# Optimization experiments

Measured on AMD Instinct MI355X. Metric: run time of the kernel, lower is better.

The kernel has to match this reference:

```python
import jax, jax.numpy as jnp
import numpy as np

N_NODES = 100000
N_EDGES = 1600000
IN_CH = 128
HID = 128
OUT_CH = 16
N_GRAPHS = 64


def setup_inputs() -> dict:
    key = jax.random.key(0)
    ks = jax.random.split(key, 8)
    x = jax.random.normal(ks[0], (N_NODES, IN_CH), dtype=jnp.float32)
    edge_index = jax.random.randint(ks[1], (2, N_EDGES), 0, N_NODES, dtype=jnp.int64)
    batch = jnp.sort(jax.random.randint(ks[2], (N_NODES,), 0, N_GRAPHS, dtype=jnp.int64))
    s1 = 1.0 / np.sqrt(IN_CH)
    s2 = 1.0 / np.sqrt(HID)
    W1 = jax.random.uniform(ks[3], (IN_CH, HID), jnp.float32, -s1, s1)
    b1 = jnp.zeros((HID,), jnp.float32)
    W2 = jax.random.uniform(ks[4], (HID, HID), jnp.float32, -s2, s2)
    b2 = jnp.zeros((HID,), jnp.float32)
    Wfc = jax.random.uniform(ks[5], (HID, OUT_CH), jnp.float32, -s2, s2)
    bfc = jax.random.uniform(ks[6], (OUT_CH,), jnp.float32, -s2, s2)
    return {"x": x, "W1": W1, "b1": b1, "W2": W2, "b2": b2,
            "Wfc": Wfc, "bfc": bfc, "edge_index": edge_index, "batch": batch}


def _gcn_conv(x, W, b, src, dst, deg_inv_sqrt, deg_inv):
    # GCNConv with self-loops: out = D^-1/2 (A+I) D^-1/2 (x W) + b
    h = x @ W                                   # [N, H]
    norm = deg_inv_sqrt[src] * deg_inv_sqrt[dst]  # [E]
    agg = jax.ops.segment_sum(h[src] * norm[:, None], dst, num_segments=N_NODES)
    # self-loop term: deg_inv_sqrt[i]^2 * h[i]
    return agg + h * deg_inv[:, None] + b


def reference(x, W1, b1, W2, b2, Wfc, bfc, edge_index, batch):
    src, dst = edge_index[0], edge_index[1]
    # degree including self-loop
    deg = jax.ops.segment_sum(jnp.ones((N_EDGES,), jnp.float32), dst, num_segments=N_NODES) + 1.0
    deg_inv_sqrt = jax.lax.rsqrt(deg)
    deg_inv = 1.0 / deg
    h = jax.nn.relu(_gcn_conv(x, W1, b1, src, dst, deg_inv_sqrt, deg_inv))
    h = jax.nn.relu(_gcn_conv(h, W2, b2, src, dst, deg_inv_sqrt, deg_inv))
    # global mean pool over graphs
    sums = jax.ops.segment_sum(h, batch, num_segments=N_GRAPHS)          # [G, H]
    counts = jax.ops.segment_sum(jnp.ones((N_NODES,), jnp.float32), batch, num_segments=N_GRAPHS)
    pooled = sums / jnp.maximum(counts, 1.0)[:, None]
    return pooled @ Wfc + bfc
```

## Files before the change

### kernel.cpp

```cpp
#include <hip/hip_runtime.h>
#include <math.h>

#define NN 100000
#define NE 1600000
#define CH 128
#define OUTC 16
#define NG 64

#define CBSH 9
#define NCB 196
#define CHK 8192
#define CAP 10240
#define MAXB 12288
#define LDSW 68

typedef __attribute__((ext_vector_type(8))) short bf16x8;
typedef __attribute__((ext_vector_type(4))) float f32x4;

__device__ __forceinline__ unsigned short f2bf(float f) {
    union { float f; unsigned u; } v; v.f = f;
    unsigned r = v.u + 0x7FFF + ((v.u >> 16) & 1);
    return (unsigned short)(r >> 16);
}
__device__ __forceinline__ float bflo(unsigned u) {
    union { unsigned u; float f; } v; v.u = u << 16; return v.f;
}
__device__ __forceinline__ float bfhi(unsigned u) {
    union { unsigned u; float f; } v; v.u = u & 0xffff0000u; return v.f;
}

__device__ __forceinline__ float2 node_agg(const unsigned* __restrict__ base,
        const int* __restrict__ rowst, const int* __restrict__ degi,
        const int* __restrict__ csr, const float* __restrict__ dis,
        float bb0, float bb1, int n, int lane) {
    unsigned sv = base[(size_t)n * 64 + lane];
    float a0[8], a1[8];
    a0[0] = bflo(sv); a1[0] = bfhi(sv);
#pragma unroll
    for (int u = 1; u < 8; u++) { a0[u] = 0.f; a1[u] = 0.f; }
    int start = __builtin_amdgcn_readfirstlane(rowst[n]);
    int c = __builtin_amdgcn_readfirstlane(degi[n]);
    int j = 0;
    for (; j + 7 < c; j += 8) {
        int idx[8];
#pragma unroll
        for (int u = 0; u < 8; u++) idx[u] = csr[start + j + u];
        unsigned v[8];
#pragma unroll
        for (int u = 0; u < 8; u++) v[u] = base[(size_t)idx[u] * 64 + lane];
#pragma unroll
        for (int u = 0; u < 8; u++) { a0[u] += bflo(v[u]); a1[u] += bfhi(v[u]); }
    }
    for (; j < c; j++) {
        unsigned v0 = base[(size_t)csr[start + j] * 64 + lane];
        a0[j & 7] += bflo(v0); a1[j & 7] += bfhi(v0);
    }
#pragma unroll
    for (int off = 4; off >= 1; off >>= 1)
#pragma unroll
        for (int u = 0; u < off; u++) { a0[u] += a0[u + off]; a1[u] += a1[u + off]; }
    float d = dis[n];
    float ox = fmaxf(fmaf(d, a0[0], bb0), 0.f);
    float oy = fmaxf(fmaf(d, a1[0], bb1), 0.f);
    return make_float2(ox, oy);
}

__global__ void k_prep(const float* __restrict__ W1, const float* __restrict__ W2,
                       unsigned short* __restrict__ wt1, unsigned short* __restrict__ wt2,
                       const int* __restrict__ batch, int* __restrict__ gptr,
                       int* __restrict__ gfill, float* __restrict__ pooled) {
    int i = blockIdx.x * 256 + threadIdx.x;
    if (i < CH * CH) {
        int k = i >> 7, n = i & 127;
        wt1[n * CH + k] = f2bf(W1[i]);
    } else if (i < 2 * CH * CH) {
        int j = i - CH * CH;
        int k = j >> 7, n = j & 127;
        wt2[n * CH + k] = f2bf(W2[j]);
    }
    if (i < NCB) gfill[i] = 0;
    if (i < NG * CH) pooled[i] = 0.f;
    if (i < NN) {
        int b = batch[i];
        int prev = (i == 0) ? -1 : batch[i - 1];
        for (int g = prev + 1; g <= b; g++) gptr[g] = i;
        if (i == NN - 1) {
            for (int g = b + 1; g <= NG; g++) gptr[g] = NN;
        }
    }
}

__global__ __launch_bounds__(1024) void k_passA(const int* __restrict__ src, const int* __restrict__ dst,
                        int* __restrict__ gfill, unsigned* __restrict__ ebuf) {
    __shared__ unsigned lbuf[CHK];
    __shared__ unsigned char lbyte[CHK];
    __shared__ int hcnt[NCB];
    __shared__ int hbase[256];
    __shared__ int goff[NCB];
    int t = threadIdx.x;
    if (t < NCB) hcnt[t] = 0;
    __syncthreads();
    int base = blockIdx.x * CHK;
    int cb[8], slot[8]; unsigned pk[8];
#pragma unroll
    for (int i = 0; i < 8; i++) {
        int e = base + i * 1024 + t;
        cb[i] = -1;
        if (e < NE) {
            int d = dst[e], s = src[e];
            cb[i] = d >> CBSH;
            pk[i] = ((unsigned)s << CBSH) | (unsigned)(d & 511);
            slot[i] = atomicAdd(&hcnt[cb[i]], 1);
        }
    }
    __syncthreads();
    if (t < 256) hbase[t] = (t < NCB) ? hcnt[t] : 0;
    __syncthreads();
    for (int off = 1; off < 256; off <<= 1) {
        int v = 0;
        if (t < 256 && t >= off) v = hbase[t - off];
        __syncthreads();
        if (t < 256) hbase[t] += v;
        __syncthreads();
    }
    if (t < NCB) {
        int c = hcnt[t];
        int g = c ? atomicAdd(&gfill[t], c) : 0;
        goff[t] = t * CAP + g - (hbase[t] - c);
    }
    __syncthreads();
#pragma unroll
    for (int i = 0; i < 8; i++) {
        if (cb[i] >= 0) {
            int pos = hbase[cb[i]] - hcnt[cb[i]] + slot[i];
            lbuf[pos] = pk[i];
            lbyte[pos] = (unsigned char)cb[i];
        }
    }
    __syncthreads();
    int total = min(NE - base, CHK);
    for (int p = t; p < total; p += 1024) {
        unsigned v = lbuf[p];
        int b = lbyte[p];
        ebuf[goff[b] + p] = v;
    }
}

__global__ __launch_bounds__(1024) void k_passB(const unsigned* __restrict__ ebuf, const int* __restrict__ gfill,
                        int* __restrict__ degi, int* __restrict__ rowst,
                        float* __restrict__ dis, int* __restrict__ csr) {
    __shared__ int cnt[512];
    __shared__ int nbase[512];
    __shared__ int fill[512];
    __shared__ int stage[MAXB];
    int t = threadIdx.x;
    int cb = blockIdx.x;
    int nb0 = cb << CBSH;
    int ncnt = min(512, NN - nb0);
    int e0 = cb * CAP;
    int e1 = e0 + gfill[cb];
    if (t < 512) { cnt[t] = 0; fill[t] = 0; }
    __syncthreads();
    for (int e = e0 + t; e < e1; e += 1024)
        atomicAdd(&cnt[ebuf[e] & 511], 1);
    __syncthreads();
    if (t < 512) nbase[t] = cnt[t];
    __syncthreads();
    for (int off = 1; off < 512; off <<= 1) {
        int v = 0;
        if (t < 512 && t >= off) v = nbase[t - off];
        __syncthreads();
        if (t < 512) nbase[t] += v;
        __syncthreads();
    }
    for (int e = e0 + t; e < e1; e += 1024) {
        unsigned v = ebuf[e];
        int local = v & 511;
        int s = atomicAdd(&fill[local], 1);
        stage[nbase[local] - cnt[local] + s] = (int)(v >> CBSH);
    }
    __syncthreads();
    int total = e1 - e0;
    for (int p = t; p < total; p += 1024) csr[e0 + p] = stage[p];
    if (t < ncnt) {
        int c = cnt[t];
        degi[nb0 + t] = c;
        rowst[nb0 + t] = e0 + nbase[t] - c;
        dis[nb0 + t] = rsqrtf((float)c + 1.0f);
    }
}

__launch_bounds__(256, 2)
__global__ void k_gemm1(const float* __restrict__ A,
                        const unsigned short* __restrict__ WT,
                        const float* __restrict__ dis,
                        unsigned short* __restrict__ out) {
    int tid = threadIdx.x;
    int wave = tid >> 6, lane = tid & 63;
    int quad = lane >> 4, l16 = lane & 15;

    int rbase = blockIdx.x * 128 + wave * 32;

    bf16x8 af[2][4];
#pragma unroll
    for (int s = 0; s < 2; s++) {
        int row = rbase + s * 16 + l16;
        if (row >= NN) row = NN - 1;
        const float* arow = A + (size_t)row * CH + quad * 8;
#pragma unroll
        for (int ks = 0; ks < 4; ks++) {
            float4 lo = *(const float4*)(arow + ks * 32);
            float4 hi = *(const float4*)(arow + ks * 32 + 4);
            union { bf16x8 v; unsigned short u[8]; } tmp;
            tmp.u[0] = f2bf(lo.x); tmp.u[1] = f2bf(lo.y);
            tmp.u[2] = f2bf(lo.z); tmp.u[3] = f2bf(lo.w);
            tmp.u[4] = f2bf(hi.x); tmp.u[5] = f2bf(hi.y);
            tmp.u[6] = f2bf(hi.z); tmp.u[7] = f2bf(hi.w);
            af[s][ks] = tmp.v;
        }
    }

    f32x4 acc[2][8];
#pragma unroll
    for (int s = 0; s < 2; s++)
#pragma unroll
        for (int t = 0; t < 8; t++) acc[s][t] = (f32x4){0.f, 0.f, 0.f, 0.f};

#pragma unroll
    for (int t = 0; t < 8; t++) {
        const unsigned short* wcol = WT + (size_t)(t * 16 + l16) * CH + quad * 8;
        bf16x8 b0 = *(const bf16x8*)(wcol);
        bf16x8 b1 = *(const bf16x8*)(wcol + 32);
        bf16x8 b2 = *(const bf16x8*)(wcol + 64);
        bf16x8 b3 = *(const bf16x8*)(wcol + 96);
#pragma unroll
        for (int s = 0; s < 2; s++) {
            acc[s][t] = __builtin_amdgcn_mfma_f32_16x16x32_bf16(af[s][0], b0, acc[s][t], 0, 0, 0);
            acc[s][t] = __builtin_amdgcn_mfma_f32_16x16x32_bf16(af[s][1], b1, acc[s][t], 0, 0, 0);
            acc[s][t] = __builtin_amdgcn_mfma_f32_16x16x32_bf16(af[s][2], b2, acc[s][t], 0, 0, 0);
            acc[s][t] = __builtin_amdgcn_mfma_f32_16x16x32_bf16(af[s][3], b3, acc[s][t], 0, 0, 0);
        }
    }

#pragma unroll
    for (int s = 0; s < 2; s++) {
#pragma unroll
        for (int r = 0; r < 4; r++) {
            int orow = rbase + s * 16 + quad * 4 + r;
            if (orow < NN) {
                float d = dis[orow];
#pragma unroll
                for (int t = 0; t < 8; t++) {
                    out[(size_t)orow * CH + t * 16 + l16] = f2bf(acc[s][t][r] * d);
                }
            }
        }
    }
}

__launch_bounds__(256)
__global__ void k_aggemm(const unsigned short* __restrict__ bufA,
                         const int* __restrict__ rowst, const int* __restrict__ degi,
                         const int* __restrict__ csr, const float* __restrict__ dis,
                         const float* __restrict__ b1,
                         const unsigned short* __restrict__ WT,
                         unsigned short* __restrict__ out) {
    __shared__ unsigned hs[128 * LDSW];
    int tid = threadIdx.x;
    int wave = tid >> 6, lane = tid & 63;
    int quad = lane >> 4, l16 = lane & 15;
    int rbase = blockIdx.x * 128 + wave * 32;
    const unsigned* base = (const unsigned*)bufA;
    float bb0 = b1[lane * 2], bb1 = b1[lane * 2 + 1];

    for (int i = 0; i < 32; i++) {
        int n = rbase + i;
        int nc = n < NN ? n : NN - 1;
        float2 o = node_agg(base, rowst, degi, csr, dis, bb0, bb1, nc, lane);
        unsigned pk = ((unsigned)f2bf(o.y) << 16) | (unsigned)f2bf(o.x);
        hs[(wave * 32 + i) * LDSW + lane] = pk;
    }
    __syncthreads();

    bf16x8 af[2][4];
#pragma unroll
    for (int s = 0; s < 2; s++) {
        int r = wave * 32 + s * 16 + l16;
#pragma unroll
        for (int ks = 0; ks < 4; ks++)
            af[s][ks] = *(const bf16x8*)&hs[r * LDSW + quad * 4 + ks * 16];
    }

    f32x4 acc[2][8];
#pragma unroll
    for (int s = 0; s < 2; s++)
#pragma unroll
        for (int t = 0; t < 8; t++) acc[s][t] = (f32x4){0.f, 0.f, 0.f, 0.f};

#pragma unroll
    for (int t = 0; t < 8; t++) {
        const unsigned short* wcol = WT + (size_t)(t * 16 + l16) * CH + quad * 8;
        bf16x8 b0 = *(const bf16x8*)(wcol);
        bf16x8 b1f = *(const bf16x8*)(wcol + 32);
        bf16x8 b2f = *(const bf16x8*)(wcol + 64);
        bf16x8 b3f = *(const bf16x8*)(wcol + 96);
#pragma unroll
        for (int s = 0; s < 2; s++) {
            acc[s][t] = __builtin_amdgcn_mfma_f32_16x16x32_bf16(af[s][0], b0,  acc[s][t], 0, 0, 0);
            acc[s][t] = __builtin_amdgcn_mfma_f32_16x16x32_bf16(af[s][1], b1f, acc[s][t], 0, 0, 0);
            acc[s][t] = __builtin_amdgcn_mfma_f32_16x16x32_bf16(af[s][2], b2f, acc[s][t], 0, 0, 0);
            acc[s][t] = __builtin_amdgcn_mfma_f32_16x16x32_bf16(af[s][3], b3f, acc[s][t], 0, 0, 0);
        }
    }

#pragma unroll
    for (int s = 0; s < 2; s++) {
#pragma unroll
        for (int r = 0; r < 4; r++) {
            int orow = rbase + s * 16 + quad * 4 + r;
            if (orow < NN) {
                float d = dis[orow];
#pragma unroll
                for (int t = 0; t < 8; t++) {
                    out[(size_t)orow * CH + t * 16 + l16] = f2bf(acc[s][t][r] * d);
                }
            }
        }
    }
}

__global__ void k_aggpool(const unsigned short* __restrict__ ht,
                          const int* __restrict__ rowst, const int* __restrict__ degi,
                          const int* __restrict__ csr, const float* __restrict__ dis,
                          const float* __restrict__ b2, const int* __restrict__ batch,
                          float* __restrict__ pooled) {
    int wave = threadIdx.x >> 6;
    int lane = threadIdx.x & 63;
    int n0 = (blockIdx.x * 4 + wave) * 32;
    if (n0 >= NN) return;
    int n1 = n0 + 32; if (n1 > NN) n1 = NN;
    const unsigned* base = (const unsigned*)ht;
    float bb0 = b2[lane * 2], bb1 = b2[lane * 2 + 1];
    float p0 = 0.f, p1 = 0.f;
    int gcur = __builtin_amdgcn_readfirstlane(batch[n0]);
    for (int n = n0; n < n1; n++) {
        int g = __builtin_amdgcn_readfirstlane(batch[n]);
        if (g != gcur) {
            atomicAdd(&pooled[gcur * CH + lane * 2],     p0);
            atomicAdd(&pooled[gcur * CH + lane * 2 + 1], p1);
            p0 = 0.f; p1 = 0.f; gcur = g;
        }
        float2 o = node_agg(base, rowst, degi, csr, dis, bb0, bb1, n, lane);
        p0 += o.x; p1 += o.y;
    }
    atomicAdd(&pooled[gcur * CH + lane * 2],     p0);
    atomicAdd(&pooled[gcur * CH + lane * 2 + 1], p1);
}

__global__ void k_final(const float* __restrict__ pooled, const int* __restrict__ gptr,
                        const float* __restrict__ Wfc, const float* __restrict__ bfc,
                        float* __restrict__ out) {
    int idx = blockIdx.x * 256 + threadIdx.x;
    if (idx >= NG * OUTC) return;
    int g = idx >> 4, o = idx & 15;
    float c = (float)(gptr[g + 1] - gptr[g]);
    float inv = 1.0f / fmaxf(c, 1.0f);
    float s = 0.f;
    for (int k = 0; k < CH; k++) s += pooled[g * CH + k] * Wfc[k * OUTC + o];
    out[idx] = fmaf(s, inv, bfc[o]);
}

extern "C" void kernel_launch(void* const* d_in, const int* in_sizes, int n_in,
                              void* d_out, int out_size, void* d_ws, size_t ws_size,
                              hipStream_t stream) {
    (void)in_sizes; (void)n_in; (void)out_size; (void)ws_size;
    const float* x   = (const float*)d_in[0];
    const float* W1  = (const float*)d_in[1];
    const float* b1  = (const float*)d_in[2];
    const float* W2  = (const float*)d_in[3];
    const float* b2  = (const float*)d_in[4];
    const float* Wfc = (const float*)d_in[5];
    const float* bfc = (const float*)d_in[6];
    const int* ei    = (const int*)d_in[7];
    const int* batch = (const int*)d_in[8];
    const int* esrc = ei;
    const int* edst = ei + NE;
    float* out = (float*)d_out;

    char* w = (char*)d_ws;
    unsigned short* bufA = (unsigned short*)w; w += (size_t)NN * CH * 2;
    unsigned short* bufB = (unsigned short*)w; w += (size_t)NN * CH * 2;
    unsigned short* wt1  = (unsigned short*)w; w += (size_t)CH * CH * 2;
    unsigned short* wt2  = (unsigned short*)w; w += (size_t)CH * CH * 2;
    unsigned* ebuf = (unsigned*)w; w += (size_t)NCB * CAP * 4;
    int* csr    = (int*)w;    w += (size_t)NCB * CAP * 4;
    int* degi   = (int*)w;    w += (size_t)NN * 4;
    int* rowst  = (int*)w;    w += (size_t)NN * 4;
    float* dis  = (float*)w;  w += (size_t)NN * 4;
    int* gfill  = (int*)w;    w += NCB * 4;
    int* gptr   = (int*)w;    w += (NG + 1) * 4;
    float* pooled = (float*)w; w += (size_t)NG * CH * 4;

    const int sortBlocks = (NE + CHK - 1) / CHK;
    const int rowBlocks  = (NN + 127) / 128;

    k_prep<<<(NN + 255) / 256, 256, 0, stream>>>(W1, W2, wt1, wt2, batch, gptr, gfill, pooled);
    k_passA<<<sortBlocks, 1024, 0, stream>>>(esrc, edst, gfill, ebuf);
    k_passB<<<NCB, 1024, 0, stream>>>(ebuf, gfill, degi, rowst, dis, csr);

    k_gemm1<<<rowBlocks, 256, 0, stream>>>(x, wt1, dis, bufA);
    k_aggemm<<<rowBlocks, 256, 0, stream>>>(bufA, rowst, degi, csr, dis, b1, wt2, bufB);
    k_aggpool<<<rowBlocks, 256, 0, stream>>>(bufB, rowst, degi, csr, dis, b2, batch, pooled);

    k_final<<<(NG * OUTC + 255) / 256, 256, 0, stream>>>(pooled, gptr, Wfc, bfc, out);
}
```

Before: 386.2 us.

## Split fused aggregate-GEMM kernel into separate per-node aggregation and bf16 GEMM

Replaces the fused layer-2 aggregation+GEMM kernel, which had each wave serially aggregate 32 nodes into LDS before running MFMA, with a standalone aggregation kernel using one wave per node, followed by a templated GEMM kernel that reads bf16 input directly. This exposes far more parallelism in the gather-heavy aggregation and removes the LDS staging and block barrier. The cost is an extra kernel launch and an extra round trip of the 100k x 128 bf16 intermediate through global memory.

```diff
diff --git a/kernel.cpp b/kernel.cpp
--- a/kernel.cpp
+++ b/kernel.cpp
@@ -12,7 +12,6 @@
 #define CHK 8192
 #define CAP 10240
 #define MAXB 12288
-#define LDSW 68
 
 typedef __attribute__((ext_vector_type(8))) short bf16x8;
 typedef __attribute__((ext_vector_type(4))) float f32x4;
@@ -190,11 +189,12 @@
     }
 }
 
+template<bool F32IN>
 __launch_bounds__(256, 2)
-__global__ void k_gemm1(const float* __restrict__ A,
-                        const unsigned short* __restrict__ WT,
-                        const float* __restrict__ dis,
-                        unsigned short* __restrict__ out) {
+__global__ void k_gemm(const void* __restrict__ Av,
+                       const unsigned short* __restrict__ WT,
+                       const float* __restrict__ dis,
+                       unsigned short* __restrict__ out) {
     int tid = threadIdx.x;
     int wave = tid >> 6, lane = tid & 63;
     int quad = lane >> 4, l16 = lane & 15;
@@ -206,17 +206,23 @@
     for (int s = 0; s < 2; s++) {
         int row = rbase + s * 16 + l16;
         if (row >= NN) row = NN - 1;
-        const float* arow = A + (size_t)row * CH + quad * 8;
-#pragma unroll
-        for (int ks = 0; ks < 4; ks++) {
-            float4 lo = *(const float4*)(arow + ks * 32);
-            float4 hi = *(const float4*)(arow + ks * 32 + 4);
-            union { bf16x8 v; unsigned short u[8]; } tmp;
-            tmp.u[0] = f2bf(lo.x); tmp.u[1] = f2bf(lo.y);
-            tmp.u[2] = f2bf(lo.z); tmp.u[3] = f2bf(lo.w);
-            tmp.u[4] = f2bf(hi.x); tmp.u[5] = f2bf(hi.y);
-            tmp.u[6] = f2bf(hi.z); tmp.u[7] = f2bf(hi.w);
-            af[s][ks] = tmp.v;
+        if (F32IN) {
+            const float* arow = (const float*)Av + (size_t)row * CH + quad * 8;
+#pragma unroll
+            for (int ks = 0; ks < 4; ks++) {
+                float4 lo = *(const float4*)(arow + ks * 32);
+                float4 hi = *(const float4*)(arow + ks * 32 + 4);
+                union { bf16x8 v; unsigned short u[8]; } tmp;
+                tmp.u[0] = f2bf(lo.x); tmp.u[1] = f2bf(lo.y);
+                tmp.u[2] = f2bf(lo.z); tmp.u[3] = f2bf(lo.w);
+                tmp.u[4] = f2bf(hi.x); tmp.u[5] = f2bf(hi.y);
+                tmp.u[6] = f2bf(hi.z); tmp.u[7] = f2bf(hi.w);
+                af[s][ks] = tmp.v;
+            }
+        } else {
+            const unsigned short* arow = (const unsigned short*)Av + (size_t)row * CH + quad * 8;
+#pragma unroll
+            for (int ks = 0; ks < 4; ks++) af[s][ks] = *(const bf16x8*)(arow + ks * 32);
         }
     }
 
@@ -258,75 +264,19 @@
     }
 }
 
-__launch_bounds__(256)
-__global__ void k_aggemm(const unsigned short* __restrict__ bufA,
-                         const int* __restrict__ rowst, const int* __restrict__ degi,
-                         const int* __restrict__ csr, const float* __restrict__ dis,
-                         const float* __restrict__ b1,
-                         const unsigned short* __restrict__ WT,
-                         unsigned short* __restrict__ out) {
-    __shared__ unsigned hs[128 * LDSW];
-    int tid = threadIdx.x;
-    int wave = tid >> 6, lane = tid & 63;
-    int quad = lane >> 4, l16 = lane & 15;
-    int rbase = blockIdx.x * 128 + wave * 32;
-    const unsigned* base = (const unsigned*)bufA;
-    float bb0 = b1[lane * 2], bb1 = b1[lane * 2 + 1];
-
-    for (int i = 0; i < 32; i++) {
-        int n = rbase + i;
-        int nc = n < NN ? n : NN - 1;
-        float2 o = node_agg(base, rowst, degi, csr, dis, bb0, bb1, nc, lane);
-        unsigned pk = ((unsigned)f2bf(o.y) << 16) | (unsigned)f2bf(o.x);
-        hs[(wave * 32 + i) * LDSW + lane] = pk;
-    }
-    __syncthreads();
-
-    bf16x8 af[2][4];
-#pragma unroll
-    for (int s = 0; s < 2; s++) {
-        int r = wave * 32 + s * 16 + l16;
-#pragma unroll
-        for (int ks = 0; ks < 4; ks++)
-            af[s][ks] = *(const bf16x8*)&hs[r * LDSW + quad * 4 + ks * 16];
-    }
-
-    f32x4 acc[2][8];
-#pragma unroll
-    for (int s = 0; s < 2; s++)
-#pragma unroll
-        for (int t = 0; t < 8; t++) acc[s][t] = (f32x4){0.f, 0.f, 0.f, 0.f};
-
-#pragma unroll
-    for (int t = 0; t < 8; t++) {
-        const unsigned short* wcol = WT + (size_t)(t * 16 + l16) * CH + quad * 8;
-        bf16x8 b0 = *(const bf16x8*)(wcol);
-        bf16x8 b1f = *(const bf16x8*)(wcol + 32);
-        bf16x8 b2f = *(const bf16x8*)(wcol + 64);
-        bf16x8 b3f = *(const bf16x8*)(wcol + 96);
-#pragma unroll
-        for (int s = 0; s < 2; s++) {
-            acc[s][t] = __builtin_amdgcn_mfma_f32_16x16x32_bf16(af[s][0], b0,  acc[s][t], 0, 0, 0);
-            acc[s][t] = __builtin_amdgcn_mfma_f32_16x16x32_bf16(af[s][1], b1f, acc[s][t], 0, 0, 0);
-            acc[s][t] = __builtin_amdgcn_mfma_f32_16x16x32_bf16(af[s][2], b2f, acc[s][t], 0, 0, 0);
-            acc[s][t] = __builtin_amdgcn_mfma_f32_16x16x32_bf16(af[s][3], b3f, acc[s][t], 0, 0, 0);
-        }
-    }
-
-#pragma unroll
-    for (int s = 0; s < 2; s++) {
-#pragma unroll
-        for (int r = 0; r < 4; r++) {
-            int orow = rbase + s * 16 + quad * 4 + r;
-            if (orow < NN) {
-                float d = dis[orow];
-#pragma unroll
-                for (int t = 0; t < 8; t++) {
-                    out[(size_t)orow * CH + t * 16 + l16] = f2bf(acc[s][t][r] * d);
-                }
-            }
-        }
-    }
+__global__ void k_agg(const unsigned short* __restrict__ ht, const int* __restrict__ rowst,
+                      const int* __restrict__ degi, const int* __restrict__ csr,
+                      const float* __restrict__ dis, const float* __restrict__ bias,
+                      unsigned short* __restrict__ out) {
+    int wave = threadIdx.x >> 6;
+    int lane = threadIdx.x & 63;
+    int n = blockIdx.x * 4 + wave;
+    if (n >= NN) return;
+    const unsigned* base = (const unsigned*)ht;
+    float bb0 = bias[lane * 2], bb1 = bias[lane * 2 + 1];
+    float2 o = node_agg(base, rowst, degi, csr, dis, bb0, bb1, n, lane);
+    unsigned pk = ((unsigned)f2bf(o.y) << 16) | (unsigned)f2bf(o.x);
+    ((unsigned*)out)[(size_t)n * 64 + lane] = pk;
 }
 
 __global__ void k_aggpool(const unsigned short* __restrict__ ht,
@@ -408,9 +358,10 @@
     k_passA<<<sortBlocks, 1024, 0, stream>>>(esrc, edst, gfill, ebuf);
     k_passB<<<NCB, 1024, 0, stream>>>(ebuf, gfill, degi, rowst, dis, csr);
 
-    k_gemm1<<<rowBlocks, 256, 0, stream>>>(x, wt1, dis, bufA);
-    k_aggemm<<<rowBlocks, 256, 0, stream>>>(bufA, rowst, degi, csr, dis, b1, wt2, bufB);
-    k_aggpool<<<rowBlocks, 256, 0, stream>>>(bufB, rowst, degi, csr, dis, b2, batch, pooled);
+    k_gemm<true><<<rowBlocks, 256, 0, stream>>>(x, wt1, dis, bufA);
+    k_agg<<<NN / 4, 256, 0, stream>>>(bufA, rowst, degi, csr, dis, b1, bufB);
+    k_gemm<false><<<rowBlocks, 256, 0, stream>>>(bufB, wt2, dis, bufA);
+    k_aggpool<<<rowBlocks, 256, 0, stream>>>(bufA, rowst, degi, csr, dis, b2, batch, pooled);
 
     k_final<<<(NG * OUTC + 255) / 256, 256, 0, stream>>>(pooled, gptr, Wfc, bfc, out);
 }
```

Measured after the change: 359.3 us. 1.07x faster.
